# Performance work log

Hardware: AMD Instinct MI355X
Metric: run time of the kernel (lower is better)

The kernel has to match this reference:

```python
import jax, jax.numpy as jnp
import numpy as np

N = 50000       # nodes
E = 800000      # edges (before self-loops)
IN_DIM = 256
HID = 64
HEADS = 3
N_CLASSES = 40
NEG_SLOPE = 0.2  # PyG GATConv default negative_slope


def setup_inputs() -> dict:
    key = jax.random.key(0)
    ks = jax.random.split(key, 12)
    x = jax.random.normal(ks[0], (N, IN_DIM), jnp.float32)
    src = jax.random.randint(ks[1], (E,), 0, N, dtype=jnp.int32)
    off = jax.random.randint(ks[2], (E,), 1, N, dtype=jnp.int32)
    dst = (src + off) % N  # guarantees no self-loops
    edge_index = jnp.stack([src, dst], axis=0)
    g = 0.1
    W1 = jax.random.normal(ks[3], (IN_DIM, HEADS * HID), jnp.float32) * g
    att_src1 = jax.random.normal(ks[4], (HEADS, HID), jnp.float32) * g
    att_dst1 = jax.random.normal(ks[5], (HEADS, HID), jnp.float32) * g
    b1 = jnp.zeros((HEADS * HID,), jnp.float32)
    W2 = jax.random.normal(ks[6], (HEADS * HID, HEADS * HID), jnp.float32) * g
    att_src2 = jax.random.normal(ks[7], (HEADS, HID), jnp.float32) * g
    att_dst2 = jax.random.normal(ks[8], (HEADS, HID), jnp.float32) * g
    b2 = jnp.zeros((HEADS * HID,), jnp.float32)
    Wout = jax.random.normal(ks[9], (HEADS * HID, N_CLASSES), jnp.float32) * g
    bout = jnp.zeros((N_CLASSES,), jnp.float32)
    return {"x": x, "edge_index": edge_index,
            "W1": W1, "att_src1": att_src1, "att_dst1": att_dst1, "b1": b1,
            "W2": W2, "att_src2": att_src2, "att_dst2": att_dst2, "b2": b2,
            "Wout": Wout, "bout": bout}


def _segment_softmax(logits, seg, num_segments):
    # logits: [E', H], seg: [E'] destination node ids
    m = jax.ops.segment_max(logits, seg, num_segments=num_segments)
    e = jnp.exp(logits - m[seg])
    s = jax.ops.segment_sum(e, seg, num_segments=num_segments)
    return e / s[seg]


def _gat_layer(x, src, dst, W, att_src, att_dst, bias):
    n = x.shape[0]
    h = (x @ W).reshape(n, HEADS, HID)               # lin_src == lin_dst (x is a Tensor)
    a_src = jnp.sum(h * att_src, axis=-1)            # [N, H]
    a_dst = jnp.sum(h * att_dst, axis=-1)            # [N, H]
    alpha = jax.nn.leaky_relu(a_src[src] + a_dst[dst], NEG_SLOPE)  # [E', H]
    alpha = _segment_softmax(alpha, dst, n)
    msg = h[src] * alpha[:, :, None]                 # [E', H, C]
    out = jax.ops.segment_sum(msg, dst, num_segments=n)  # scatter-add aggregate
    return out.reshape(n, HEADS * HID) + bias        # concat heads + bias


def reference(x, edge_index, W1, att_src1, att_dst1, b1,
              W2, att_src2, att_dst2, b2, Wout, bout):
    n = x.shape[0]
    loop = jnp.arange(n, dtype=edge_index.dtype)
    src = jnp.concatenate([edge_index[0], loop])     # add_self_loops=True
    dst = jnp.concatenate([edge_index[1], loop])
    h = _gat_layer(x, src, dst, W1, att_src1, att_dst1, b1)
    h = jax.nn.relu(h)                               # dropout p=0 -> identity
    h = _gat_layer(h, src, dst, W2, att_src2, att_dst2, b2)
    h = jax.nn.relu(h)
    return h @ Wout + bout                           # node-level readout + outlayer
```

## Files before the change

### kernel.cpp

```cpp
#include <hip/hip_runtime.h>
#include <math.h>

#define NN 50000
#define NE 800000
#define KIN 256
#define F 192
#define NH 3
#define NC 40
#define NBLK 49
#define CNT_BLKS ((NE+255)/256)
#define CONV_N (F*KIN + F*F + 48*F)
#define CONV_BLKS ((CONV_N+255)/256)

typedef unsigned short u16;
typedef unsigned int   u32;
typedef __attribute__((ext_vector_type(8))) short bf16x8;
typedef __attribute__((ext_vector_type(4))) float f32x4;

static __device__ __forceinline__ u16 f2bf(float f){
  u32 u = __float_as_uint(f);
  u32 r = (u + 0x7fffu + ((u >> 16) & 1u)) >> 16;
  return (u16)r;
}

__global__ void count_conv_kernel(const int* __restrict__ dst, int* __restrict__ cnt,
                                  const float* __restrict__ W1, const float* __restrict__ W2,
                                  const float* __restrict__ Wout,
                                  u16* __restrict__ w1t, u16* __restrict__ w2t, u16* __restrict__ wot){
  int b = blockIdx.x;
  if (b < CNT_BLKS){
    int e = b*256 + threadIdx.x;
    if (e < NE) atomicAdd(&cnt[dst[e]], 1);
    return;
  }
  int e = (b - CNT_BLKS)*256 + threadIdx.x;
  if (e < F*KIN){
    int c = e / KIN, r = e % KIN;
    w1t[e] = f2bf(W1[(size_t)r*F + c]);
    return;
  }
  int e2 = e - F*KIN;
  if (e2 < F*F){
    int c = e2 / F, r = e2 % F;
    w2t[e2] = f2bf(W2[(size_t)r*F + c]);
    return;
  }
  int e3 = e2 - F*F;
  if (e3 < 48*F){
    int n = e3 / F, k = e3 % F;
    wot[e3] = (n < NC)? f2bf(Wout[(size_t)k*NC + n]) : (u16)0;
  }
}

__global__ __launch_bounds__(256) void partial_kernel(const int* __restrict__ cnt, int* __restrict__ partials){
  __shared__ int red[256];
  const int t = threadIdx.x;
  const int base = blockIdx.x*1024 + t*4;
  int s = 0;
  if (base + 3 < NN){
    int4 v = *(const int4*)&cnt[base];
    s = v.x + v.y + v.z + v.w;
  } else if (base < NN){
    for (int i=base; i<NN; i++) s += cnt[i];
  }
  red[t] = s;
  __syncthreads();
  for (int off=128; off; off>>=1){
    if (t < off) red[t] += red[t+off];
    __syncthreads();
  }
  if (t==0) partials[blockIdx.x] = red[0];
}

__global__ __launch_bounds__(64) void scan_partials(const int* __restrict__ partials,
                                                    int* __restrict__ offsets, int* __restrict__ row_ptr){
  const int lane = threadIdx.x;
  int p = (lane < NBLK)? partials[lane] : 0;
  int inc = p;
  #pragma unroll
  for (int off=1; off<64; off<<=1){
    int v = __shfl_up(inc, off);
    if (lane >= off) inc += v;
  }
  if (lane < NBLK) offsets[lane] = inc - p;
  if (lane == NBLK-1) row_ptr[NN] = inc;
}

__global__ __launch_bounds__(256) void emit_kernel(int* __restrict__ cnt,
                                                   const int* __restrict__ offsets,
                                                   int* __restrict__ row_ptr){
  __shared__ int ts[256];
  const int t = threadIdx.x;
  const int base = blockIdx.x*1024 + t*4;
  int4 v = make_int4(0,0,0,0);
  if (base + 3 < NN) v = *(const int4*)&cnt[base];
  else if (base < NN){
    v.x = cnt[base];
    if (base+1 < NN) v.y = cnt[base+1];
    if (base+2 < NN) v.z = cnt[base+2];
  }
  int tot = v.x + v.y + v.z + v.w;
  ts[t] = tot;
  __syncthreads();
  #pragma unroll
  for (int off=1; off<256; off<<=1){
    int val = (t >= off)? ts[t-off] : 0;
    __syncthreads();
    ts[t] += val;
    __syncthreads();
  }
  int off0 = offsets[blockIdx.x] + ts[t] - tot;
  if (base + 3 < NN){
    row_ptr[base]   = off0;
    row_ptr[base+1] = off0 + v.x;
    row_ptr[base+2] = off0 + v.x + v.y;
    row_ptr[base+3] = off0 + v.x + v.y + v.z;
    *(int4*)&cnt[base] = make_int4(0,0,0,0);
  } else if (base < NN){
    row_ptr[base] = off0; cnt[base] = 0;
    if (base+1 < NN){ row_ptr[base+1] = off0 + v.x; cnt[base+1] = 0; }
    if (base+2 < NN){ row_ptr[base+2] = off0 + v.x + v.y; cnt[base+2] = 0; }
  }
}

__global__ void fill_kernel(const int* __restrict__ src, const int* __restrict__ dst,
                            const int* __restrict__ row_ptr, int* __restrict__ cur,
                            int* __restrict__ col){
  int e = blockIdx.x*256 + threadIdx.x;
  if (e < NE){
    int d = dst[e];
    int p = row_ptr[d] + atomicAdd(&cur[d], 1);
    col[p] = src[e];
  }
}

#define SAK 72
#define SC  196
template<int K, bool CONVA>
__global__ __launch_bounds__(256) void gemm_mfma(const void* __restrict__ Araw, const u16* __restrict__ Bt,
                                                 u16* __restrict__ C,
                                                 const float* __restrict__ att_src, const float* __restrict__ att_dst,
                                                 float* __restrict__ a_src4, float* __restrict__ a_dst4){
  __shared__ __align__(16) union {
    struct { u16 As[64*SAK]; u16 Bs[192*SAK]; } st;
    u16 Cs[64*SC];
  } sh;
  const int t = threadIdx.x;
  const int wave = t >> 6, lane = t & 63;
  const int quad = lane >> 4, l16 = lane & 15;
  const int r0 = blockIdx.x*64;

  f32x4 acc[4][3];
  #pragma unroll
  for (int rt=0;rt<4;rt++)
    #pragma unroll
    for (int ct=0;ct<3;ct++) acc[rt][ct] = (f32x4){0.f,0.f,0.f,0.f};

  for (int k0=0; k0<K; k0+=64){
    __syncthreads();
    {
      int row = t >> 2, kq = (t & 3)*16;
      bool ok = (r0+row) < NN;
      if (CONVA){
        const float* Af = (const float*)Araw;
        float4 v0 = make_float4(0,0,0,0), v1 = v0, v2 = v0, v3 = v0;
        if (ok){
          const float* p = &Af[(size_t)(r0+row)*K + k0 + kq];
          v0 = *(const float4*)(p+0);
          v1 = *(const float4*)(p+4);
          v2 = *(const float4*)(p+8);
          v3 = *(const float4*)(p+12);
        }
        uint4 pa, pb;
        pa.x = (u32)f2bf(v0.x) | ((u32)f2bf(v0.y) << 16);
        pa.y = (u32)f2bf(v0.z) | ((u32)f2bf(v0.w) << 16);
        pa.z = (u32)f2bf(v1.x) | ((u32)f2bf(v1.y) << 16);
        pa.w = (u32)f2bf(v1.z) | ((u32)f2bf(v1.w) << 16);
        pb.x = (u32)f2bf(v2.x) | ((u32)f2bf(v2.y) << 16);
        pb.y = (u32)f2bf(v2.z) | ((u32)f2bf(v2.w) << 16);
        pb.z = (u32)f2bf(v3.x) | ((u32)f2bf(v3.y) << 16);
        pb.w = (u32)f2bf(v3.z) | ((u32)f2bf(v3.w) << 16);
        *(uint4*)&sh.st.As[row*SAK + kq]     = pa;
        *(uint4*)&sh.st.As[row*SAK + kq + 8] = pb;
      } else {
        const u16* Ab = (const u16*)Araw;
        uint4 va = make_uint4(0,0,0,0), vb = va;
        if (ok){
          va = *(const uint4*)&Ab[(size_t)(r0+row)*K + k0 + kq];
          vb = *(const uint4*)&Ab[(size_t)(r0+row)*K + k0 + kq + 8];
        }
        *(uint4*)&sh.st.As[row*SAK + kq]     = va;
        *(uint4*)&sh.st.As[row*SAK + kq + 8] = vb;
      }
    }
    #pragma unroll
    for (int i=0;i<6;i++){
      int idx = t + i*256;
      int n = idx >> 3, kc = idx & 7;
      *(uint4*)&sh.st.Bs[n*SAK + kc*8] = *(const uint4*)&Bt[(size_t)n*K + k0 + kc*8];
    }
    __syncthreads();
    bf16x8 af[4][2], bf[3][2];
    #pragma unroll
    for (int kf=0;kf<2;kf++){
      #pragma unroll
      for (int rt=0;rt<4;rt++) af[rt][kf] = *(const bf16x8*)&sh.st.As[(rt*16 + l16)*SAK + kf*32 + quad*8];
      #pragma unroll
      for (int ct=0;ct<3;ct++) bf[ct][kf] = *(const bf16x8*)&sh.st.Bs[(wave*48 + ct*16 + l16)*SAK + kf*32 + quad*8];
    }
    #pragma unroll
    for (int kf=0;kf<2;kf++)
      #pragma unroll
      for (int rt=0;rt<4;rt++)
        #pragma unroll
        for (int ct=0;ct<3;ct++)
          acc[rt][ct] = __builtin_amdgcn_mfma_f32_16x16x32_bf16(af[rt][kf], bf[ct][kf], acc[rt][ct], 0, 0, 0);
  }

  __syncthreads();
  #pragma unroll
  for (int ct=0;ct<3;ct++){
    const int n = wave*48 + ct*16 + l16;
    #pragma unroll
    for (int rt=0;rt<4;rt++){
      #pragma unroll
      for (int reg=0;reg<4;reg++){
        const int m = rt*16 + quad*4 + reg;
        sh.Cs[m*SC + n] = f2bf(acc[rt][ct][reg]);
      }
    }
  }
  __syncthreads();
  {
    int row = t >> 2, c0 = (t & 3)*6;
    int grow = r0 + row;
    if (grow < NN){
      #pragma unroll
      for (int j=0;j<6;j++){
        int ch = c0 + j;
        uint4 v = *(const uint4*)&sh.Cs[row*SC + ch*8];
        *(uint4*)&C[(size_t)grow*F + ch*8] = v;
      }
    }
  }
  if (t < 192){
    int row = t & 63, head = t >> 6;
    int grow = r0 + row;
    if (grow < NN){
      float ps = 0.f, pd = 0.f;
      #pragma unroll
      for (int j=0;j<8;j++){
        uint4 v = *(const uint4*)&sh.Cs[row*SC + head*64 + j*8];
        float4 w0 = *(const float4*)&att_src[head*64 + j*8];
        float4 w1 = *(const float4*)&att_src[head*64 + j*8 + 4];
        float4 d0 = *(const float4*)&att_dst[head*64 + j*8];
        float4 d1 = *(const float4*)&att_dst[head*64 + j*8 + 4];
        float c0f = __uint_as_float(v.x << 16), c1f = __uint_as_float(v.x & 0xffff0000u);
        float c2f = __uint_as_float(v.y << 16), c3f = __uint_as_float(v.y & 0xffff0000u);
        float c4f = __uint_as_float(v.z << 16), c5f = __uint_as_float(v.z & 0xffff0000u);
        float c6f = __uint_as_float(v.w << 16), c7f = __uint_as_float(v.w & 0xffff0000u);
        ps = fmaf(c0f,w0.x,fmaf(c1f,w0.y,fmaf(c2f,w0.z,fmaf(c3f,w0.w,ps))));
        ps = fmaf(c4f,w1.x,fmaf(c5f,w1.y,fmaf(c6f,w1.z,fmaf(c7f,w1.w,ps))));
        pd = fmaf(c0f,d0.x,fmaf(c1f,d0.y,fmaf(c2f,d0.z,fmaf(c3f,d0.w,pd))));
        pd = fmaf(c4f,d1.x,fmaf(c5f,d1.y,fmaf(c6f,d1.z,fmaf(c7f,d1.w,pd))));
      }
      a_src4[(size_t)grow*4 + head] = ps;
      a_dst4[(size_t)grow*4 + head] = pd;
    }
  }
}

__global__ __launch_bounds__(256) void gat_agg_wave(const u16* __restrict__ hb,
    const float* __restrict__ a_src4, const float* __restrict__ a_dst4,
    const int* __restrict__ row_ptr, const int* __restrict__ col,
    const float* __restrict__ bias, u16* __restrict__ out){
  __shared__ float s_al[4][64][4];
  const int t = threadIdx.x;
  const int lane = t & 63;
  const int w = t >> 6;
  const int d = blockIdx.x*4 + w;
  if (d >= NN) return;
  const int e0  = row_ptr[d];
  const int deg = row_ptr[d+1] - e0;
  const int ecount = deg + 1;
  const float4 ad = *(const float4*)&a_dst4[(size_t)d*4];

  const int cg = (lane < 48)? lane : lane - 48;
  const int hg = (lane < 48)? (lane >> 4) : 0;
  const int cgo = cg*4;
  float4 acc = make_float4(0.f,0.f,0.f,0.f);
  float sl0=0.f, sl1=0.f, sl2=0.f;

  for (int base=0; base<ecount; base+=64){
    int j = base + lane;
    bool valid = j < ecount;
    int sn = d;
    if (j < deg) sn = col[e0+j];
    float4 as = *(const float4*)&a_src4[(size_t)sn*4];
    float l0 = as.x + ad.x; l0 = (l0>0.f)? l0 : 0.2f*l0;
    float l1 = as.y + ad.y; l1 = (l1>0.f)? l1 : 0.2f*l1;
    float l2 = as.z + ad.z; l2 = (l2>0.f)? l2 : 0.2f*l2;
    float E0 = valid? __expf(l0) : 0.f;
    float E1 = valid? __expf(l1) : 0.f;
    float E2 = valid? __expf(l2) : 0.f;
    sl0 += E0; sl1 += E1; sl2 += E2;
    float4 st; st.x = E0; st.y = E1; st.z = E2; st.w = 0.f;
    *(float4*)&s_al[w][lane][0] = st;
    __builtin_amdgcn_wave_barrier();
    int cnt = ecount - base; if (cnt > 64) cnt = 64;
    int jj = 0;
    for (; jj+4 <= cnt; jj += 4){
      int sA = __builtin_amdgcn_readlane(sn, jj);
      int sB = __builtin_amdgcn_readlane(sn, jj+1);
      int sC = __builtin_amdgcn_readlane(sn, jj+2);
      int sD = __builtin_amdgcn_readlane(sn, jj+3);
      uint2 pA = *(const uint2*)(hb + sA*F + cgo);
      uint2 pB = *(const uint2*)(hb + sB*F + cgo);
      uint2 pC = *(const uint2*)(hb + sC*F + cgo);
      uint2 pD = *(const uint2*)(hb + sD*F + cgo);
      float aA = s_al[w][jj  ][hg];
      float aB = s_al[w][jj+1][hg];
      float aC = s_al[w][jj+2][hg];
      float aD = s_al[w][jj+3][hg];
      acc.x = fmaf(aA, __uint_as_float(pA.x << 16),         acc.x);
      acc.y = fmaf(aA, __uint_as_float(pA.x & 0xffff0000u), acc.y);
      acc.z = fmaf(aA, __uint_as_float(pA.y << 16),         acc.z);
      acc.w = fmaf(aA, __uint_as_float(pA.y & 0xffff0000u), acc.w);
      acc.x = fmaf(aB, __uint_as_float(pB.x << 16),         acc.x);
      acc.y = fmaf(aB, __uint_as_float(pB.x & 0xffff0000u), acc.y);
      acc.z = fmaf(aB, __uint_as_float(pB.y << 16),         acc.z);
      acc.w = fmaf(aB, __uint_as_float(pB.y & 0xffff0000u), acc.w);
      acc.x = fmaf(aC, __uint_as_float(pC.x << 16),         acc.x);
      acc.y = fmaf(aC, __uint_as_float(pC.x & 0xffff0000u), acc.y);
      acc.z = fmaf(aC, __uint_as_float(pC.y << 16),         acc.z);
      acc.w = fmaf(aC, __uint_as_float(pC.y & 0xffff0000u), acc.w);
      acc.x = fmaf(aD, __uint_as_float(pD.x << 16),         acc.x);
      acc.y = fmaf(aD, __uint_as_float(pD.x & 0xffff0000u), acc.y);
      acc.z = fmaf(aD, __uint_as_float(pD.y << 16),         acc.z);
      acc.w = fmaf(aD, __uint_as_float(pD.y & 0xffff0000u), acc.w);
    }
    for (; jj < cnt; jj++){
      int sA = __builtin_amdgcn_readlane(sn, jj);
      uint2 pA = *(const uint2*)(hb + sA*F + cgo);
      float aA = s_al[w][jj][hg];
      acc.x = fmaf(aA, __uint_as_float(pA.x << 16),         acc.x);
      acc.y = fmaf(aA, __uint_as_float(pA.x & 0xffff0000u), acc.y);
      acc.z = fmaf(aA, __uint_as_float(pA.y << 16),         acc.z);
      acc.w = fmaf(aA, __uint_as_float(pA.y & 0xffff0000u), acc.w);
    }
    __builtin_amdgcn_wave_barrier();
  }
  #pragma unroll
  for (int off=32; off; off>>=1){
    sl0 += __shfl_xor(sl0, off);
    sl1 += __shfl_xor(sl1, off);
    sl2 += __shfl_xor(sl2, off);
  }
  if (lane < 48){
    float inv = 1.f / ((hg==0)? sl0 : ((hg==1)? sl1 : sl2));
    float4 b4 = *(const float4*)&bias[cg*4];
    uint2 o;
    o.x = (u32)f2bf(fmaxf(fmaf(acc.x, inv, b4.x), 0.f))
        | ((u32)f2bf(fmaxf(fmaf(acc.y, inv, b4.y), 0.f)) << 16);
    o.y = (u32)f2bf(fmaxf(fmaf(acc.z, inv, b4.z), 0.f))
        | ((u32)f2bf(fmaxf(fmaf(acc.w, inv, b4.w), 0.f)) << 16);
    *(uint2*)&out[(size_t)d*F + cg*4] = o;
  }
}

__global__ __launch_bounds__(256) void gemm_out_mfma(const u16* __restrict__ A,
    const u16* __restrict__ Wt, const float* __restrict__ bias, float* __restrict__ out){
  const int t = threadIdx.x;
  const int wave = t >> 6, lane = t & 63;
  const int quad = lane >> 4, l16 = lane & 15;
  const int rbase = blockIdx.x*64 + wave*16;
  const int arow = rbase + l16;
  f32x4 acc[3];
  #pragma unroll
  for (int ct=0;ct<3;ct++) acc[ct] = (f32x4){0.f,0.f,0.f,0.f};
  #pragma unroll
  for (int ks=0; ks<6; ks++){
    const int k0 = ks*32;
    union { uint4 u; bf16x8 h; } cva;
    cva.u = make_uint4(0,0,0,0);
    if (arow < NN) cva.u = *(const uint4*)&A[(size_t)arow*F + k0 + quad*8];
    #pragma unroll
    for (int ct=0;ct<3;ct++){
      bf16x8 bfr = *(const bf16x8*)&Wt[(size_t)(ct*16 + l16)*F + k0 + quad*8];
      acc[ct] = __builtin_amdgcn_mfma_f32_16x16x32_bf16(cva.h, bfr, acc[ct], 0, 0, 0);
    }
  }
  #pragma unroll
  for (int ct=0;ct<3;ct++){
    const int n = ct*16 + l16;
    #pragma unroll
    for (int reg=0;reg<4;reg++){
      const int m = quad*4 + reg;
      const int grow = rbase + m;
      if (grow < NN && n < NC) out[(size_t)grow*NC + n] = acc[ct][reg] + bias[n];
    }
  }
}

extern "C" void kernel_launch(void* const* d_in, const int* in_sizes, int n_in,
                              void* d_out, int out_size, void* d_ws, size_t ws_size,
                              hipStream_t stream){
  const float* x    = (const float*)d_in[0];
  const int*   ei   = (const int*)  d_in[1];
  const float* W1   = (const float*)d_in[2];
  const float* as1  = (const float*)d_in[3];
  const float* ad1  = (const float*)d_in[4];
  const float* b1   = (const float*)d_in[5];
  const float* W2   = (const float*)d_in[6];
  const float* as2  = (const float*)d_in[7];
  const float* ad2  = (const float*)d_in[8];
  const float* b2   = (const float*)d_in[9];
  const float* Wout = (const float*)d_in[10];
  const float* bout = (const float*)d_in[11];
  float* out = (float*)d_out;

  u16* w1t = (u16*)d_ws;
  u16* w2t = w1t + (size_t)F*KIN;
  u16* wot = w2t + (size_t)F*F;
  u16* hb1 = wot + (size_t)48*F;
  u16* hb2 = hb1 + (size_t)NN*F;
  u16* gb1 = hb2 + (size_t)NN*F;
  u16* gb2 = gb1 + (size_t)NN*F;
  float* a_src4 = (float*)(gb2 + (size_t)NN*F);
  float* a_dst4 = a_src4 + (size_t)NN*4;
  int* row_ptr  = (int*)(a_dst4 + (size_t)NN*4);
  int* col      = row_ptr + (NN+1);
  int* cnt      = col + NE;
  int* partials = cnt + NN;
  int* offsets  = partials + NBLK;

  const int* srcv = ei;
  const int* dstv = ei + NE;

  hipMemsetAsync(cnt, 0, NN*sizeof(int), stream);
  count_conv_kernel<<<CNT_BLKS + CONV_BLKS, 256, 0, stream>>>(dstv, cnt, W1, W2, Wout, w1t, w2t, wot);
  partial_kernel<<<NBLK, 256, 0, stream>>>(cnt, partials);
  scan_partials<<<1, 64, 0, stream>>>(partials, offsets, row_ptr);
  emit_kernel<<<NBLK, 256, 0, stream>>>(cnt, offsets, row_ptr);
  fill_kernel<<<(NE+255)/256, 256, 0, stream>>>(srcv, dstv, row_ptr, cnt, col);

  const int GEMM_GRID = (NN + 63)/64;
  const int AGG_GRID  = (NN + 3)/4;
  gemm_mfma<KIN,true><<<GEMM_GRID, 256, 0, stream>>>(x, w1t, hb1, as1, ad1, a_src4, a_dst4);
  gat_agg_wave<<<AGG_GRID, 256, 0, stream>>>(hb1, a_src4, a_dst4, row_ptr, col, b1, gb1);
  gemm_mfma<F,false><<<GEMM_GRID, 256, 0, stream>>>(gb1, w2t, hb2, as2, ad2, a_src4, a_dst4);
  gat_agg_wave<<<AGG_GRID, 256, 0, stream>>>(hb2, a_src4, a_dst4, row_ptr, col, b2, gb2);
  gemm_out_mfma<<<GEMM_GRID, 256, 0, stream>>>(gb2, wot, bout, out);
}
```

Measured before the change: 343.5 us.

## Fuse CSR build into one persistent kernel with software grid barriers

Replaces the five CSR-construction and weight-conversion kernels with one persistent 256-block kernel. The count, scan, offset, emit and fill phases are separated by atomic-counter grid barriers. The aim is to cut kernel launch overhead and inter-kernel gaps in the preprocessing stage. It depends on all 256 blocks being resident at once, and it adds spin-wait and serialized single-block scan costs.

```diff
diff --git a/kernel.cpp b/kernel.cpp
--- a/kernel.cpp
+++ b/kernel.cpp
@@ -7,10 +7,10 @@
 #define F 192
 #define NH 3
 #define NC 40
-#define NBLK 49
-#define CNT_BLKS ((NE+255)/256)
 #define CONV_N (F*KIN + F*F + 48*F)
-#define CONV_BLKS ((CONV_N+255)/256)
+#define CSR_BLKS 256
+#define CHUNK 196
+#define EPB (NE/CSR_BLKS)
 
 typedef unsigned short u16;
 typedef unsigned int   u32;
@@ -23,114 +23,97 @@
   return (u16)r;
 }
 
-__global__ void count_conv_kernel(const int* __restrict__ dst, int* __restrict__ cnt,
-                                  const float* __restrict__ W1, const float* __restrict__ W2,
-                                  const float* __restrict__ Wout,
-                                  u16* __restrict__ w1t, u16* __restrict__ w2t, u16* __restrict__ wot){
-  int b = blockIdx.x;
-  if (b < CNT_BLKS){
-    int e = b*256 + threadIdx.x;
-    if (e < NE) atomicAdd(&cnt[dst[e]], 1);
-    return;
-  }
-  int e = (b - CNT_BLKS)*256 + threadIdx.x;
-  if (e < F*KIN){
-    int c = e / KIN, r = e % KIN;
-    w1t[e] = f2bf(W1[(size_t)r*F + c]);
-    return;
-  }
-  int e2 = e - F*KIN;
-  if (e2 < F*F){
-    int c = e2 / F, r = e2 % F;
-    w2t[e2] = f2bf(W2[(size_t)r*F + c]);
-    return;
-  }
-  int e3 = e2 - F*F;
-  if (e3 < 48*F){
-    int n = e3 / F, k = e3 % F;
-    wot[e3] = (n < NC)? f2bf(Wout[(size_t)k*NC + n]) : (u16)0;
-  }
-}
-
-__global__ __launch_bounds__(256) void partial_kernel(const int* __restrict__ cnt, int* __restrict__ partials){
-  __shared__ int red[256];
-  const int t = threadIdx.x;
-  const int base = blockIdx.x*1024 + t*4;
-  int s = 0;
-  if (base + 3 < NN){
-    int4 v = *(const int4*)&cnt[base];
-    s = v.x + v.y + v.z + v.w;
-  } else if (base < NN){
-    for (int i=base; i<NN; i++) s += cnt[i];
-  }
-  red[t] = s;
+static __device__ __forceinline__ void gbar(int* bar, int target){
   __syncthreads();
-  for (int off=128; off; off>>=1){
-    if (t < off) red[t] += red[t+off];
+  if (threadIdx.x == 0){
+    __threadfence();
+    atomicAdd(bar, 1);
+    while (__hip_atomic_load(bar, __ATOMIC_ACQUIRE, __HIP_MEMORY_SCOPE_AGENT) < target){
+      __builtin_amdgcn_s_sleep(8);
+    }
+  }
+  __syncthreads();
+  __threadfence();
+}
+
+__global__ __launch_bounds__(256) void csr_build(
+    const int* __restrict__ src, const int* __restrict__ dst,
+    int* cnt, int* bar, int* partials, int* offsets, int* row_ptr, int* __restrict__ col,
+    const float* __restrict__ W1, const float* __restrict__ W2, const float* __restrict__ Wout,
+    u16* __restrict__ w1t, u16* __restrict__ w2t, u16* __restrict__ wot){
+  const int b = blockIdx.x, t = threadIdx.x;
+  const int gid = b*256 + t;
+  __shared__ int ts[256];
+
+  for (int e = gid; e < CONV_N; e += CSR_BLKS*256){
+    if (e < F*KIN){
+      int c = e / KIN, r = e % KIN;
+      w1t[e] = f2bf(W1[(size_t)r*F + c]);
+    } else if (e < F*KIN + F*F){
+      int e2 = e - F*KIN;
+      int c = e2 / F, r = e2 % F;
+      w2t[e2] = f2bf(W2[(size_t)r*F + c]);
+    } else {
+      int e3 = e - F*KIN - F*F;
+      int n = e3 / F, k = e3 % F;
+      wot[e3] = (n < NC)? f2bf(Wout[(size_t)k*NC + n]) : (u16)0;
+    }
+  }
+  {
+    const int e0 = b*EPB;
+    for (int i = t; i < EPB; i += 256)
+      atomicAdd(&cnt[dst[e0+i]], 1);
+  }
+  gbar(bar, CSR_BLKS);
+
+  const int base = b*CHUNK;
+  int v = 0;
+  if (t < CHUNK && base+t < NN) v = cnt[base+t];
+  int incl = v;
+  ts[t] = incl;
+  __syncthreads();
+  #pragma unroll
+  for (int off=1; off<256; off<<=1){
+    int u = (t>=off)? ts[t-off] : 0;
     __syncthreads();
-  }
-  if (t==0) partials[blockIdx.x] = red[0];
-}
-
-__global__ __launch_bounds__(64) void scan_partials(const int* __restrict__ partials,
-                                                    int* __restrict__ offsets, int* __restrict__ row_ptr){
-  const int lane = threadIdx.x;
-  int p = (lane < NBLK)? partials[lane] : 0;
-  int inc = p;
-  #pragma unroll
-  for (int off=1; off<64; off<<=1){
-    int v = __shfl_up(inc, off);
-    if (lane >= off) inc += v;
-  }
-  if (lane < NBLK) offsets[lane] = inc - p;
-  if (lane == NBLK-1) row_ptr[NN] = inc;
-}
-
-__global__ __launch_bounds__(256) void emit_kernel(int* __restrict__ cnt,
-                                                   const int* __restrict__ offsets,
-                                                   int* __restrict__ row_ptr){
-  __shared__ int ts[256];
-  const int t = threadIdx.x;
-  const int base = blockIdx.x*1024 + t*4;
-  int4 v = make_int4(0,0,0,0);
-  if (base + 3 < NN) v = *(const int4*)&cnt[base];
-  else if (base < NN){
-    v.x = cnt[base];
-    if (base+1 < NN) v.y = cnt[base+1];
-    if (base+2 < NN) v.z = cnt[base+2];
-  }
-  int tot = v.x + v.y + v.z + v.w;
-  ts[t] = tot;
-  __syncthreads();
-  #pragma unroll
-  for (int off=1; off<256; off<<=1){
-    int val = (t >= off)? ts[t-off] : 0;
+    incl += u;
+    ts[t] = incl;
     __syncthreads();
-    ts[t] += val;
+  }
+  if (t == 255) partials[b] = incl;
+  gbar(bar, 2*CSR_BLKS);
+
+  if (b == 0){
+    int p = partials[t];
+    int inc2 = p;
+    ts[t] = inc2;
     __syncthreads();
-  }
-  int off0 = offsets[blockIdx.x] + ts[t] - tot;
-  if (base + 3 < NN){
-    row_ptr[base]   = off0;
-    row_ptr[base+1] = off0 + v.x;
-    row_ptr[base+2] = off0 + v.x + v.y;
-    row_ptr[base+3] = off0 + v.x + v.y + v.z;
-    *(int4*)&cnt[base] = make_int4(0,0,0,0);
-  } else if (base < NN){
-    row_ptr[base] = off0; cnt[base] = 0;
-    if (base+1 < NN){ row_ptr[base+1] = off0 + v.x; cnt[base+1] = 0; }
-    if (base+2 < NN){ row_ptr[base+2] = off0 + v.x + v.y; cnt[base+2] = 0; }
-  }
-}
-
-__global__ void fill_kernel(const int* __restrict__ src, const int* __restrict__ dst,
-                            const int* __restrict__ row_ptr, int* __restrict__ cur,
-                            int* __restrict__ col){
-  int e = blockIdx.x*256 + threadIdx.x;
-  if (e < NE){
-    int d = dst[e];
-    int p = row_ptr[d] + atomicAdd(&cur[d], 1);
-    col[p] = src[e];
+    #pragma unroll
+    for (int off=1; off<256; off<<=1){
+      int u = (t>=off)? ts[t-off] : 0;
+      __syncthreads();
+      inc2 += u;
+      ts[t] = inc2;
+      __syncthreads();
+    }
+    offsets[t] = inc2 - p;
+    if (t == 255) row_ptr[NN] = inc2;
+  }
+  gbar(bar, 3*CSR_BLKS);
+
+  if (t < CHUNK && base+t < NN){
+    row_ptr[base+t] = offsets[b] + incl - v;
+    cnt[base+t] = 0;
+  }
+  gbar(bar, 4*CSR_BLKS);
+
+  {
+    const int e0 = b*EPB;
+    for (int i = t; i < EPB; i += 256){
+      int d = dst[e0+i];
+      int p = row_ptr[d] + atomicAdd(&cnt[d], 1);
+      col[p] = src[e0+i];
+    }
   }
 }
 
@@ -431,18 +414,16 @@
   int* row_ptr  = (int*)(a_dst4 + (size_t)NN*4);
   int* col      = row_ptr + (NN+1);
   int* cnt      = col + NE;
-  int* partials = cnt + NN;
-  int* offsets  = partials + NBLK;
+  int* bar      = cnt + NN;
+  int* partials = bar + 1;
+  int* offsets  = partials + CSR_BLKS;
 
   const int* srcv = ei;
   const int* dstv = ei + NE;
 
-  hipMemsetAsync(cnt, 0, NN*sizeof(int), stream);
-  count_conv_kernel<<<CNT_BLKS + CONV_BLKS, 256, 0, stream>>>(dstv, cnt, W1, W2, Wout, w1t, w2t, wot);
-  partial_kernel<<<NBLK, 256, 0, stream>>>(cnt, partials);
-  scan_partials<<<1, 64, 0, stream>>>(partials, offsets, row_ptr);
-  emit_kernel<<<NBLK, 256, 0, stream>>>(cnt, offsets, row_ptr);
-  fill_kernel<<<(NE+255)/256, 256, 0, stream>>>(srcv, dstv, row_ptr, cnt, col);
+  hipMemsetAsync(cnt, 0, (NN+1)*sizeof(int), stream);
+  csr_build<<<CSR_BLKS, 256, 0, stream>>>(srcv, dstv, cnt, bar, partials, offsets,
+                                          row_ptr, col, W1, W2, Wout, w1t, w2t, wot);
 
   const int GEMM_GRID = (NN + 63)/64;
   const int AGG_GRID  = (NN + 3)/4;
```

Measured after the change: 463.2 us. +34.8%, slower.

## Merge CSR scan kernels into one and fold edge fill into first GEMM

Applied to the files above, without the earlier changes.

Replaces the three-kernel scan (partial sums, scan of partials, emit) with a single kernel in which each block recomputes the sum of all counts before its range. It also appends the CSR fill blocks to the first GEMM launch as extra blocks, so the fill runs alongside the GEMM. This removes three kernel launches and their serialization gaps. In exchange, later blocks redundantly read up to the whole count array, and the fill blocks compete with GEMM blocks for compute units.

```diff
diff --git a/kernel.cpp b/kernel.cpp
--- a/kernel.cpp
+++ b/kernel.cpp
@@ -7,10 +7,11 @@
 #define F 192
 #define NH 3
 #define NC 40
-#define NBLK 49
 #define CNT_BLKS ((NE+255)/256)
 #define CONV_N (F*KIN + F*F + 48*F)
 #define CONV_BLKS ((CONV_N+255)/256)
+#define GEMM_GRID_C ((NN+63)/64)
+#define EMIT_BLKS 49
 
 typedef unsigned short u16;
 typedef unsigned int   u32;
@@ -52,46 +53,25 @@
   }
 }
 
-__global__ __launch_bounds__(256) void partial_kernel(const int* __restrict__ cnt, int* __restrict__ partials){
-  __shared__ int red[256];
-  const int t = threadIdx.x;
-  const int base = blockIdx.x*1024 + t*4;
-  int s = 0;
-  if (base + 3 < NN){
-    int4 v = *(const int4*)&cnt[base];
-    s = v.x + v.y + v.z + v.w;
-  } else if (base < NN){
-    for (int i=base; i<NN; i++) s += cnt[i];
-  }
-  red[t] = s;
+__global__ __launch_bounds__(256) void emit_all(int* __restrict__ cnt, int* __restrict__ row_ptr){
+  __shared__ int ts[256];
+  __shared__ int s_pred;
+  const int b = blockIdx.x, t = threadIdx.x;
+  const int lim = b*1024;
+  int pred = 0;
+  for (int i = t*4; i < lim; i += 1024){
+    int4 v = *(const int4*)&cnt[i];
+    pred += v.x + v.y + v.z + v.w;
+  }
+  ts[t] = pred;
   __syncthreads();
   for (int off=128; off; off>>=1){
-    if (t < off) red[t] += red[t+off];
+    if (t < off) ts[t] += ts[t+off];
     __syncthreads();
   }
-  if (t==0) partials[blockIdx.x] = red[0];
-}
-
-__global__ __launch_bounds__(64) void scan_partials(const int* __restrict__ partials,
-                                                    int* __restrict__ offsets, int* __restrict__ row_ptr){
-  const int lane = threadIdx.x;
-  int p = (lane < NBLK)? partials[lane] : 0;
-  int inc = p;
-  #pragma unroll
-  for (int off=1; off<64; off<<=1){
-    int v = __shfl_up(inc, off);
-    if (lane >= off) inc += v;
-  }
-  if (lane < NBLK) offsets[lane] = inc - p;
-  if (lane == NBLK-1) row_ptr[NN] = inc;
-}
-
-__global__ __launch_bounds__(256) void emit_kernel(int* __restrict__ cnt,
-                                                   const int* __restrict__ offsets,
-                                                   int* __restrict__ row_ptr){
-  __shared__ int ts[256];
-  const int t = threadIdx.x;
-  const int base = blockIdx.x*1024 + t*4;
+  if (t == 0) s_pred = ts[0];
+  __syncthreads();
+  const int base = lim + t*4;
   int4 v = make_int4(0,0,0,0);
   if (base + 3 < NN) v = *(const int4*)&cnt[base];
   else if (base < NN){
@@ -109,7 +89,7 @@
     ts[t] += val;
     __syncthreads();
   }
-  int off0 = offsets[blockIdx.x] + ts[t] - tot;
+  int off0 = s_pred + ts[t] - tot;
   if (base + 3 < NN){
     row_ptr[base]   = off0;
     row_ptr[base+1] = off0 + v.x;
@@ -121,26 +101,28 @@
     if (base+1 < NN){ row_ptr[base+1] = off0 + v.x; cnt[base+1] = 0; }
     if (base+2 < NN){ row_ptr[base+2] = off0 + v.x + v.y; cnt[base+2] = 0; }
   }
-}
-
-__global__ void fill_kernel(const int* __restrict__ src, const int* __restrict__ dst,
-                            const int* __restrict__ row_ptr, int* __restrict__ cur,
-                            int* __restrict__ col){
-  int e = blockIdx.x*256 + threadIdx.x;
-  if (e < NE){
-    int d = dst[e];
-    int p = row_ptr[d] + atomicAdd(&cur[d], 1);
-    col[p] = src[e];
-  }
+  if (b == 0 && t == 0) row_ptr[NN] = NE;
 }
 
 #define SAK 72
 #define SC  196
-template<int K, bool CONVA>
+template<int K, bool CONVA, bool FILL>
 __global__ __launch_bounds__(256) void gemm_mfma(const void* __restrict__ Araw, const u16* __restrict__ Bt,
                                                  u16* __restrict__ C,
                                                  const float* __restrict__ att_src, const float* __restrict__ att_dst,
-                                                 float* __restrict__ a_src4, float* __restrict__ a_dst4){
+                                                 float* __restrict__ a_src4, float* __restrict__ a_dst4,
+                                                 const int* __restrict__ fsrc, const int* __restrict__ fdst,
+                                                 const int* __restrict__ row_ptr, int* __restrict__ cur,
+                                                 int* __restrict__ col){
+  if (FILL && blockIdx.x >= GEMM_GRID_C){
+    int e = (blockIdx.x - GEMM_GRID_C)*256 + threadIdx.x;
+    if (e < NE){
+      int d = fdst[e];
+      int p = row_ptr[d] + atomicAdd(&cur[d], 1);
+      col[p] = fsrc[e];
+    }
+    return;
+  }
   __shared__ __align__(16) union {
     struct { u16 As[64*SAK]; u16 Bs[192*SAK]; } st;
     u16 Cs[64*SC];
@@ -431,24 +413,20 @@
   int* row_ptr  = (int*)(a_dst4 + (size_t)NN*4);
   int* col      = row_ptr + (NN+1);
   int* cnt      = col + NE;
-  int* partials = cnt + NN;
-  int* offsets  = partials + NBLK;
 
   const int* srcv = ei;
   const int* dstv = ei + NE;
 
   hipMemsetAsync(cnt, 0, NN*sizeof(int), stream);
   count_conv_kernel<<<CNT_BLKS + CONV_BLKS, 256, 0, stream>>>(dstv, cnt, W1, W2, Wout, w1t, w2t, wot);
-  partial_kernel<<<NBLK, 256, 0, stream>>>(cnt, partials);
-  scan_partials<<<1, 64, 0, stream>>>(partials, offsets, row_ptr);
-  emit_kernel<<<NBLK, 256, 0, stream>>>(cnt, offsets, row_ptr);
-  fill_kernel<<<(NE+255)/256, 256, 0, stream>>>(srcv, dstv, row_ptr, cnt, col);
-
-  const int GEMM_GRID = (NN + 63)/64;
-  const int AGG_GRID  = (NN + 3)/4;
-  gemm_mfma<KIN,true><<<GEMM_GRID, 256, 0, stream>>>(x, w1t, hb1, as1, ad1, a_src4, a_dst4);
+  emit_all<<<EMIT_BLKS, 256, 0, stream>>>(cnt, row_ptr);
+
+  const int AGG_GRID = (NN + 3)/4;
+  gemm_mfma<KIN,true,true><<<GEMM_GRID_C + CNT_BLKS, 256, 0, stream>>>(
+      x, w1t, hb1, as1, ad1, a_src4, a_dst4, srcv, dstv, row_ptr, cnt, col);
   gat_agg_wave<<<AGG_GRID, 256, 0, stream>>>(hb1, a_src4, a_dst4, row_ptr, col, b1, gb1);
-  gemm_mfma<F,false><<<GEMM_GRID, 256, 0, stream>>>(gb1, w2t, hb2, as2, ad2, a_src4, a_dst4);
+  gemm_mfma<F,false,false><<<GEMM_GRID_C, 256, 0, stream>>>(
+      gb1, w2t, hb2, as2, ad2, a_src4, a_dst4, nullptr, nullptr, nullptr, nullptr, nullptr);
   gat_agg_wave<<<AGG_GRID, 256, 0, stream>>>(hb2, a_src4, a_dst4, row_ptr, col, b2, gb2);
-  gemm_out_mfma<<<GEMM_GRID, 256, 0, stream>>>(gb2, wot, bout, out);
-}
+  gemm_out_mfma<<<GEMM_GRID_C, 256, 0, stream>>>(gb2, wot, bout, out);
+}
```

After: 338.5 us. No clear change (-1.4%).
